# Kernel tuning notes

Measured on AMD Instinct MI355X. Metric: run time of the kernel, lower is better.

## Reference

```python
import jax, jax.numpy as jnp
import numpy as np

N = 8192      # number of tree nodes
IN = 1024     # in_dim
M = 1024      # effective mem_dim = 2 * mem_dim_init
K = 8         # max children (complete 8-ary tree)


def _linear_init(key, out_dim, in_dim):
    k1, k2 = jax.random.split(key)
    s = 1.0 / np.sqrt(in_dim)
    w = jax.random.uniform(k1, (out_dim, in_dim), minval=-s, maxval=s, dtype=jnp.float32)
    b = jax.random.uniform(k2, (out_dim,), minval=-s, maxval=s, dtype=jnp.float32)
    return w, b


def setup_inputs() -> dict:
    key = jax.random.key(0)
    ks = jax.random.split(key, 5)
    w_ioux, b_ioux = _linear_init(ks[0], 3 * M, IN)
    w_iouh, b_iouh = _linear_init(ks[1], 3 * M, M)
    w_fx, b_fx = _linear_init(ks[2], M, IN)
    w_fh, b_fh = _linear_init(ks[3], M, M)
    inputs = jax.random.normal(ks[4], (N, IN), dtype=jnp.float32)
    # Complete K-ary tree: children of node p are p*K+1 .. p*K+K (clipped).
    # Pad with index N, which addresses an always-zero dummy row.
    ch = np.full((N, K), N, dtype=np.int32)
    for j in range(K):
        idx = np.arange(N) * K + 1 + j
        valid = idx < N
        ch[valid, j] = idx[valid]
    return dict(inputs=inputs, children=jnp.asarray(ch),
                w_ioux=w_ioux, b_ioux=b_ioux, w_iouh=w_iouh, b_iouh=b_iouh,
                w_fx=w_fx, b_fx=b_fx, w_fh=w_fh, b_fh=b_fh)


def reference(inputs, children, w_ioux, b_ioux, w_iouh, b_iouh, w_fx, b_fx, w_fh, b_fh):
    # Precompute the input-side projections for all nodes at once.
    iou_x = inputs @ w_ioux.T + b_ioux   # [N, 3M]
    fx_x = inputs @ w_fx.T + b_fx        # [N, M]
    h0 = jnp.zeros((N + 1, M), inputs.dtype)  # row N is the zero pad slot
    c0 = jnp.zeros((N + 1, M), inputs.dtype)

    def step(carry, t):
        h_buf, c_buf = carry
        ch = children[t]           # [K] child indices (pad = N -> zero rows)
        ch_h = h_buf[ch]           # [K, M] real child h's
        ch_c = c_buf[ch]           # [K, M] real child c's
        # Faithful to original: for internal nodes child_c/child_h are SWAPPED,
        # so the 'child_h_sum' and f-gate inputs use the real c's, while the
        # forgotten memory (fc) multiplies the real h's. Leaves: all zeros.
        csum = ch_c.sum(0)                                   # [M]
        iou = iou_x[t] + csum @ w_iouh.T + b_iouh            # [3M]
        i_g, o_g, u_g = jnp.split(iou, 3)
        i_g = jax.nn.sigmoid(i_g)
        o_g = jax.nn.sigmoid(o_g)
        u_g = jnp.tanh(u_g)
        f = jax.nn.sigmoid(ch_c @ w_fh.T + b_fh + fx_x[t])   # [K, M]
        c = i_g * u_g + (f * ch_h).sum(0)                    # [M]
        h = o_g * jnp.tanh(c)
        return (h_buf.at[t].set(h), c_buf.at[t].set(c)), None

    # Children always have larger indices than their parent, so processing
    # t = N-1 .. 0 matches the original reverse-BFS (leaves-first) order.
    order = jnp.arange(N - 1, -1, -1)
    (h_buf, c_buf), _ = jax.lax.scan(step, (h0, c0), order)
    root_h = h_buf[0][None, :]   # [1, M]
    root_c = c_buf[0][None, :]   # [1, M]
    return root_h, root_c
```

## Files before the change

kernel.cpp:

```cpp
#include <hip/hip_runtime.h>

typedef __bf16 bf16x8 __attribute__((ext_vector_type(8)));
typedef __attribute__((ext_vector_type(4))) float f4;

#define AS1 __attribute__((address_space(1)))
#define AS3 __attribute__((address_space(3)))

__device__ __forceinline__ unsigned short f2bf(float f) {
    union { float f; unsigned int u; } x; x.f = f;
    return (unsigned short)((x.u + 0x7fffu + ((x.u >> 16) & 1u)) >> 16);
}
__device__ __forceinline__ float bf2f(unsigned short u) {
    union { unsigned int u; float f; } x; x.u = (unsigned int)u << 16;
    return x.f;
}
__device__ __forceinline__ float fsigm(float x) {
    return __builtin_amdgcn_rcpf(1.f + __expf(-x));
}
__device__ __forceinline__ float ftanh(float x) {
    return 1.f - 2.f * __builtin_amdgcn_rcpf(1.f + __expf(2.f * x));
}
__device__ __forceinline__ void gload_lds16(const unsigned short* g, unsigned short* l) {
    __builtin_amdgcn_global_load_lds((const AS1 unsigned int*)g, (AS3 unsigned int*)l, 16, 0, 0);
}
__device__ __forceinline__ void bar() {
    asm volatile("" ::: "memory");
    __builtin_amdgcn_s_barrier();
    asm volatile("" ::: "memory");
}

__global__ void prep_all_k(const float* __restrict__ inputs, const float* __restrict__ w_ioux,
                           const float* __restrict__ w_fx, const float* __restrict__ w_iouh,
                           const float* __restrict__ w_fh,
                           const float* __restrict__ b_ioux, const float* __restrict__ b_iouh,
                           const float* __restrict__ b_fx, const float* __restrict__ b_fh,
                           unsigned short* __restrict__ Xbf, unsigned short* __restrict__ Wiouxbf,
                           unsigned short* __restrict__ Wfxbf, unsigned short* __restrict__ Whbf,
                           unsigned short* __restrict__ Wfhbf,
                           float* __restrict__ bias_iou, float* __restrict__ bias_f,
                           unsigned short* __restrict__ c_bf, unsigned short* __restrict__ h_bf) {
    int b = blockIdx.x;
    if (b < 16384) {
        int idx = b * 256 + threadIdx.x;
        const float* src; unsigned short* dst; int rel;
        if (idx < 2097152)      { src = inputs; dst = Xbf;     rel = idx; }
        else if (idx < 2883584) { src = w_ioux; dst = Wiouxbf; rel = idx - 2097152; }
        else if (idx < 3145728) { src = w_fx;   dst = Wfxbf;   rel = idx - 2883584; }
        else if (idx < 3932160) { src = w_iouh; dst = Whbf;    rel = idx - 3145728; }
        else                    { src = w_fh;   dst = Wfhbf;   rel = idx - 3932160; }
        float4 v = reinterpret_cast<const float4*>(src)[rel];
        ushort4 o; o.x = f2bf(v.x); o.y = f2bf(v.y); o.z = f2bf(v.z); o.w = f2bf(v.w);
        reinterpret_cast<ushort4*>(dst)[rel] = o;
    } else if (b < 16400) {
        int idx = (b - 16384) * 256 + threadIdx.x;
        if (idx < 3072) bias_iou[idx] = b_ioux[idx] + b_iouh[idx];
        else { int j = idx - 3072; bias_f[j] = b_fx[j] + b_fh[j]; }
    } else {
        int j = (b - 16400) * 256 + threadIdx.x;
        size_t o = (size_t)8192 * 1024 + j;
        c_bf[o] = 0; h_bf[o] = 0;
    }
}

__device__ __forceinline__ void stage_half(const unsigned short* __restrict__ G, int M,
                                           int trow0, int kt, unsigned short* lds_region, int tid) {
#pragma unroll
    for (int ii = 0; ii < 2; ++ii) {
        int c = ii * 512 + tid;
        int r = c >> 3, sl = c & 7;
        int row = min(trow0 + r, M - 1);
        gload_lds16(G + (size_t)row * 1024 + kt * 64 + ((sl ^ (r & 7)) * 8),
                    lds_region + c * 8);
    }
}
__device__ __forceinline__ bf16x8 rdfrag(const unsigned short* region, int rowih, int kslot) {
    return *reinterpret_cast<const bf16x8*>(&region[rowih * 64 + ((kslot ^ (rowih & 7)) * 8)]);
}

#define RD_A(AF, REG, FB)                                                        \
    _Pragma("unroll") for (int f_ = 0; f_ < 4; ++f_)                             \
    _Pragma("unroll") for (int s_ = 0; s_ < 2; ++s_)                             \
        (AF)[f_][s_] = rdfrag((REG), ((FB) + f_) * 16 + fr, s_ * 4 + q);
#define RD_B(BQ, REG, GB)                                                        \
    _Pragma("unroll") for (int g_ = 0; g_ < 2; ++g_)                             \
    _Pragma("unroll") for (int s_ = 0; s_ < 2; ++s_)                             \
        (BQ)[g_][s_] = rdfrag((REG), bcol0 + ((GB) + g_) * 16 + fr, s_ * 4 + q);
#define MF16(FB, GB, AF, BQ)                                                     \
    __builtin_amdgcn_s_setprio(1);                                               \
    _Pragma("unroll") for (int s_ = 0; s_ < 2; ++s_)                             \
    _Pragma("unroll") for (int f_ = 0; f_ < 4; ++f_)                             \
    _Pragma("unroll") for (int g_ = 0; g_ < 2; ++g_)                             \
        acc[(FB) + f_][(GB) + g_] = __builtin_amdgcn_mfma_f32_16x16x32_bf16(     \
            (AF)[f_][s_], (BQ)[g_][s_], acc[(FB) + f_][(GB) + g_], 0, 0, 0);     \
    __builtin_amdgcn_s_setprio(0);

__device__ __forceinline__ void gemm256_core(const unsigned short* __restrict__ Am,
                                             const unsigned short* __restrict__ Bm,
                                             int M, int tm, int tn,
                                             unsigned short* ls, f4 acc[8][4]) {
    const int tid = threadIdx.x;
    const int l = tid & 63, w = tid >> 6;
    const int wm = w >> 2, wn = w & 3;
    const int fr = l & 15, q = l >> 4;
    const int bcol0 = (wn & 1) * 64;
    const int BIGM = 1 << 30;

    unsigned short* S0 = ls;
    unsigned short* S1 = ls + 32768;
    const unsigned short* Ar0 = S0 + wm * 8192;
    const unsigned short* Br0 = S0 + (2 + (wn >> 1)) * 8192;
    const unsigned short* Ar1 = S1 + wm * 8192;
    const unsigned short* Br1 = S1 + (2 + (wn >> 1)) * 8192;

#pragma unroll
    for (int i = 0; i < 8; ++i)
#pragma unroll
        for (int j = 0; j < 4; ++j) acc[i][j] = (f4){0.f, 0.f, 0.f, 0.f};

    stage_half(Am, M, tm,       0, S0 + 0 * 8192, tid);
    stage_half(Am, M, tm + 128, 0, S0 + 1 * 8192, tid);
    stage_half(Bm, BIGM, tn,       0, S0 + 2 * 8192, tid);
    stage_half(Bm, BIGM, tn + 128, 0, S0 + 3 * 8192, tid);
    stage_half(Bm, BIGM, tn,       1, S1 + 2 * 8192, tid);
    stage_half(Bm, BIGM, tn + 128, 1, S1 + 3 * 8192, tid);
    asm volatile("s_waitcnt vmcnt(4)" ::: "memory");
    bar();

    for (int i = 0; i < 8; ++i) {
        bf16x8 afA[4][2], afB[4][2], bq01[2][2], bq23[2][2];
        RD_A(afA, Ar0, 0)
        RD_B(bq01, Br0, 0)
        stage_half(Am, M, tm,       2 * i + 1, S1 + 0 * 8192, tid);
        bar();
        MF16(0, 0, afA, bq01)
        bar();
        RD_B(bq23, Br0, 2)
        stage_half(Am, M, tm + 128, 2 * i + 1, S1 + 1 * 8192, tid);
        bar();
        MF16(0, 2, afA, bq23)
        bar();
        RD_A(afB, Ar0, 4)
        if (i < 7) stage_half(Bm, BIGM, tn,       2 * i + 2, S0 + 2 * 8192, tid);
        bar();
        MF16(4, 2, afB, bq23)
        bar();
        if (i < 7) {
            stage_half(Bm, BIGM, tn + 128, 2 * i + 2, S0 + 3 * 8192, tid);
            asm volatile("s_waitcnt vmcnt(4)" ::: "memory");
        } else {
            asm volatile("s_waitcnt vmcnt(0)" ::: "memory");
        }
        bar();
        MF16(4, 0, afB, bq01)
        bar();
        RD_A(afA, Ar1, 0)
        RD_B(bq01, Br1, 0)
        if (i < 7) stage_half(Am, M, tm,       2 * i + 2, S0 + 0 * 8192, tid);
        bar();
        MF16(0, 0, afA, bq01)
        bar();
        RD_B(bq23, Br1, 2)
        if (i < 7) stage_half(Am, M, tm + 128, 2 * i + 2, S0 + 1 * 8192, tid);
        bar();
        MF16(0, 2, afA, bq23)
        bar();
        RD_A(afB, Ar1, 4)
        if (i < 7) stage_half(Bm, BIGM, tn,       2 * i + 3, S1 + 2 * 8192, tid);
        bar();
        MF16(4, 2, afB, bq23)
        bar();
        if (i < 7) {
            stage_half(Bm, BIGM, tn + 128, 2 * i + 3, S1 + 3 * 8192, tid);
            asm volatile("s_waitcnt vmcnt(4)" ::: "memory");
        } else {
            asm volatile("s_waitcnt vmcnt(0)" ::: "memory");
        }
        bar();
        MF16(4, 0, afB, bq01)
        bar();
    }
}

__global__ __launch_bounds__(512, 2)
void gemm_big_k(const unsigned short* __restrict__ Xbf, const unsigned short* __restrict__ Wioux,
                const unsigned short* __restrict__ Wfx,
                const float* __restrict__ bias_iou, const float* __restrict__ bias_f,
                unsigned short* __restrict__ P_iou, unsigned short* __restrict__ P_f) {
    __shared__ unsigned short ls[65536];
    int b = blockIdx.x;
    b = (b & 7) * 50 + (b >> 3);
    const unsigned short* Bm; unsigned short* Cp; const float* biasp;
    int tm, tn, ldc;
    if (b < 384) {
        int st = b / 24, wt = b % 24;
        tm = ((st >> 2) * 8 + wt / 3) * 256;
        tn = ((st & 3) * 3 + wt % 3) * 256;
        Bm = Wioux; Cp = P_iou; biasp = bias_iou; ldc = 3072;
    } else {
        int bb = b - 384;
        tm = (bb & 3) * 256; tn = (bb >> 2) * 256;
        Bm = Wfx; Cp = P_f; biasp = bias_f; ldc = 1024;
    }
    f4 acc[8][4];
    gemm256_core(Xbf, Bm, 8192, tm, tn, ls, acc);

    const int l = threadIdx.x & 63, w = threadIdx.x >> 6;
    const int wm = w >> 2, wn = w & 3;
    const int fr = l & 15, q = l >> 4;
#pragma unroll
    for (int f = 0; f < 8; ++f)
#pragma unroll
        for (int g = 0; g < 4; ++g) {
            int col = tn + wn * 64 + g * 16 + fr;
            float bv = biasp[col];
#pragma unroll
            for (int r = 0; r < 4; ++r) {
                int row = tm + wm * 128 + f * 16 + q * 4 + r;
                Cp[(size_t)row * ldc + col] = f2bf(acc[f][g][r] + bv);
            }
        }
}

struct LDesc {
    const unsigned short* A;
    const unsigned short* B;
    float* C;
    int M;
    int tiles_n;
    int ldc;
    int tiles_total;
};

__global__ __launch_bounds__(512, 2)
void gemm_lvl_k(LDesc d0, LDesc d1) {
    __shared__ unsigned short ls[65536];
    int b = blockIdx.x;
    LDesc d; int bb;
    if (b < d0.tiles_total) { d = d0; bb = b; }
    else { d = d1; bb = b - d0.tiles_total; }
    const int tm = (bb / d.tiles_n) * 256;
    const int tn = (bb % d.tiles_n) * 256;
    f4 acc[8][4];
    gemm256_core(d.A, d.B, d.M, tm, tn, ls, acc);

    const int l = threadIdx.x & 63, w = threadIdx.x >> 6;
    const int wm = w >> 2, wn = w & 3;
    const int fr = l & 15, q = l >> 4;
#pragma unroll
    for (int f = 0; f < 8; ++f)
#pragma unroll
        for (int g = 0; g < 4; ++g) {
            int col = tn + wn * 64 + g * 16 + fr;
#pragma unroll
            for (int r = 0; r < 4; ++r) {
                int row = tm + wm * 128 + f * 16 + q * 4 + r;
                if (row < d.M) d.C[(size_t)row * d.ldc + col] = acc[f][g][r];
            }
        }
}

__device__ __forceinline__ void gemm_core_db(const unsigned short* __restrict__ A,
                                             const unsigned short* __restrict__ B,
                                             int M, int tile_m, int tile_n, int kb, int nsteps,
                                             unsigned short* lsA, unsigned short* lsB,
                                             f4 acc[4][4]) {
    const int K = 1024;
    const int tid = threadIdx.x;
    const int l = tid & 63, wid = tid >> 6;
    const int wm = wid >> 1, wn = wid & 1;
    const int fr = l & 15, q = l >> 4;

#pragma unroll
    for (int i = 0; i < 4; ++i)
#pragma unroll
        for (int j = 0; j < 4; ++j) acc[i][j] = (f4){0.f, 0.f, 0.f, 0.f};

    const unsigned short* ga[4]; const unsigned short* gb[4];
    unsigned short *la[4], *lb[4];
#pragma unroll
    for (int i = 0; i < 4; ++i) {
        int chunk = i * 256 + tid;
        int row = chunk >> 3, slot = chunk & 7;
        int scol = (slot ^ (row & 7)) * 8;
        ga[i] = A + (size_t)min(tile_m + row, M - 1) * K + kb * 64 + scol;
        gb[i] = B + (size_t)(tile_n + row) * K + kb * 64 + scol;
        la[i] = lsA + chunk * 8;
        lb[i] = lsB + chunk * 8;
    }
#pragma unroll
    for (int i = 0; i < 4; ++i) gload_lds16(ga[i], la[i]);
#pragma unroll
    for (int i = 0; i < 4; ++i) gload_lds16(gb[i], lb[i]);

    int roffA[4], roffB[4];
#pragma unroll
    for (int f = 0; f < 4; ++f) {
        roffA[f] = (wm * 64 + f * 16 + fr) * 64;
        roffB[f] = (wn * 64 + f * 16 + fr) * 64;
    }
    const int sw = fr & 7;
    int cur = 0;
    for (int t = 0; t < nsteps; ++t) {
        if (t < nsteps - 1) {
            int k0 = (t + 1) * 64;
            int nb = (cur ^ 1) * 8192;
#pragma unroll
            for (int i = 0; i < 4; ++i) gload_lds16(ga[i] + k0, la[i] + nb);
#pragma unroll
            for (int i = 0; i < 4; ++i) gload_lds16(gb[i] + k0, lb[i] + nb);
            asm volatile("s_waitcnt vmcnt(8)" ::: "memory");
        } else {
            asm volatile("s_waitcnt vmcnt(0)" ::: "memory");
        }
        __builtin_amdgcn_s_barrier();
        const unsigned short* bA = lsA + cur * 8192;
        const unsigned short* bB = lsB + cur * 8192;
        bf16x8 af[4][2], bq[4][2];
#pragma unroll
        for (int f = 0; f < 4; ++f)
#pragma unroll
            for (int s = 0; s < 2; ++s) {
                int sl = ((s * 4 + q) ^ sw) * 8;
                af[f][s] = *reinterpret_cast<const bf16x8*>(&bA[roffA[f] + sl]);
                bq[f][s] = *reinterpret_cast<const bf16x8*>(&bB[roffB[f] + sl]);
            }
#pragma unroll
        for (int s = 0; s < 2; ++s)
#pragma unroll
            for (int i = 0; i < 4; ++i)
#pragma unroll
                for (int j = 0; j < 4; ++j)
                    acc[i][j] = __builtin_amdgcn_mfma_f32_16x16x32_bf16(af[i][s], bq[j][s], acc[i][j], 0, 0, 0);
        __builtin_amdgcn_s_barrier();
        cur ^= 1;
    }
}

__global__ void leaf_act_k(const unsigned short* __restrict__ P_iou,
                           unsigned short* __restrict__ h_bf, unsigned short* __restrict__ c_bf) {
    int idx = blockIdx.x * blockDim.x + threadIdx.x;
    int t = 1024 + (idx >> 8);
    int j = (idx & 255) * 4;
    const unsigned short* p = P_iou + (size_t)t * 3072 + j;
    ushort4 pi = *reinterpret_cast<const ushort4*>(p);
    ushort4 po = *reinterpret_cast<const ushort4*>(p + 1024);
    ushort4 pu = *reinterpret_cast<const ushort4*>(p + 2048);
    ushort4 cb, hb;
    float c0, c1, c2, c3;
    c0 = fsigm(bf2f(pi.x)) * ftanh(bf2f(pu.x)); hb.x = f2bf(fsigm(bf2f(po.x)) * ftanh(c0)); cb.x = f2bf(c0);
    c1 = fsigm(bf2f(pi.y)) * ftanh(bf2f(pu.y)); hb.y = f2bf(fsigm(bf2f(po.y)) * ftanh(c1)); cb.y = f2bf(c1);
    c2 = fsigm(bf2f(pi.z)) * ftanh(bf2f(pu.z)); hb.z = f2bf(fsigm(bf2f(po.z)) * ftanh(c2)); cb.z = f2bf(c2);
    c3 = fsigm(bf2f(pi.w)) * ftanh(bf2f(pu.w)); hb.w = f2bf(fsigm(bf2f(po.w)) * ftanh(c3)); cb.w = f2bf(c3);
    size_t o = (size_t)t * 1024 + j;
    *reinterpret_cast<ushort4*>(c_bf + o) = cb;
    *reinterpret_cast<ushort4*>(h_bf + o) = hb;
}

__device__ __forceinline__ void csum_dev(const unsigned short* __restrict__ c_bf,
                                         unsigned short* __restrict__ csum_bf, int lo, int w) {
    int tt = w >> 8, j = (w & 255) * 4;
    int t = lo + tt;
    size_t base = (size_t)(t * 8 + 1) * 1024 + j;
    float s0 = 0.f, s1 = 0.f, s2 = 0.f, s3 = 0.f;
#pragma unroll
    for (int k = 0; k < 8; ++k) {
        ushort4 v = *reinterpret_cast<const ushort4*>(c_bf + base + (size_t)k * 1024);
        s0 += bf2f(v.x); s1 += bf2f(v.y); s2 += bf2f(v.z); s3 += bf2f(v.w);
    }
    ushort4 o; o.x = f2bf(s0); o.y = f2bf(s1); o.z = f2bf(s2); o.w = f2bf(s3);
    *reinterpret_cast<ushort4*>(csum_bf + (size_t)t * 1024 + j) = o;
}

__global__ void csum_k(const unsigned short* __restrict__ c_bf, unsigned short* __restrict__ csum_bf,
                       int lo, int n) {
    int w = blockIdx.x * blockDim.x + threadIdx.x;
    if (w < n * 256) csum_dev(c_bf, csum_bf, lo, w);
}

__global__ void node_update_k(const unsigned short* __restrict__ P_iou,
                              const unsigned short* __restrict__ P_f,
                              const float* __restrict__ out_iouh, const float* __restrict__ out_f,
                              unsigned short* __restrict__ h_bf, unsigned short* __restrict__ c_bf,
                              float* __restrict__ out, int lo, int n) {
    int w = blockIdx.x * blockDim.x + threadIdx.x;
    if (w >= n * 256) return;
    int tt = w >> 8, j = (w & 255) * 4;
    int t = lo + tt;
    const unsigned short* p = P_iou + (size_t)t * 3072 + j;
    ushort4 pi4 = *reinterpret_cast<const ushort4*>(p);
    ushort4 po4 = *reinterpret_cast<const ushort4*>(p + 1024);
    ushort4 pu4 = *reinterpret_cast<const ushort4*>(p + 2048);
    const float* oi = out_iouh + (size_t)tt * 3072 + j;
    f4 oii = *reinterpret_cast<const f4*>(oi);
    f4 oio = *reinterpret_cast<const f4*>(oi + 1024);
    f4 oiu = *reinterpret_cast<const f4*>(oi + 2048);
    ushort4 pf4 = *reinterpret_cast<const ushort4*>(P_f + (size_t)t * 1024 + j);
    float pf[4] = {bf2f(pf4.x), bf2f(pf4.y), bf2f(pf4.z), bf2f(pf4.w)};
    float a[4], og[4];
    a[0] = fsigm(bf2f(pi4.x) + oii[0]) * ftanh(bf2f(pu4.x) + oiu[0]);
    a[1] = fsigm(bf2f(pi4.y) + oii[1]) * ftanh(bf2f(pu4.y) + oiu[1]);
    a[2] = fsigm(bf2f(pi4.z) + oii[2]) * ftanh(bf2f(pu4.z) + oiu[2]);
    a[3] = fsigm(bf2f(pi4.w) + oii[3]) * ftanh(bf2f(pu4.w) + oiu[3]);
    og[0] = fsigm(bf2f(po4.x) + oio[0]);
    og[1] = fsigm(bf2f(po4.y) + oio[1]);
    og[2] = fsigm(bf2f(po4.z) + oio[2]);
    og[3] = fsigm(bf2f(po4.w) + oio[3]);
#pragma unroll
    for (int k = 0; k < 8; ++k) {
        f4 fo = *reinterpret_cast<const f4*>(out_f + (size_t)(tt * 8 + k) * 1024 + j);
        ushort4 hc = *reinterpret_cast<const ushort4*>(h_bf + (size_t)(t * 8 + 1 + k) * 1024 + j);
        a[0] += fsigm(pf[0] + fo[0]) * bf2f(hc.x);
        a[1] += fsigm(pf[1] + fo[1]) * bf2f(hc.y);
        a[2] += fsigm(pf[2] + fo[2]) * bf2f(hc.z);
        a[3] += fsigm(pf[3] + fo[3]) * bf2f(hc.w);
    }
    float h0 = og[0] * ftanh(a[0]);
    float h1 = og[1] * ftanh(a[1]);
    float h2 = og[2] * ftanh(a[2]);
    float h3 = og[3] * ftanh(a[3]);
    size_t o = (size_t)t * 1024 + j;
    ushort4 cb; cb.x = f2bf(a[0]); cb.y = f2bf(a[1]); cb.z = f2bf(a[2]); cb.w = f2bf(a[3]);
    ushort4 hb; hb.x = f2bf(h0); hb.y = f2bf(h1); hb.z = f2bf(h2); hb.w = f2bf(h3);
    *reinterpret_cast<ushort4*>(c_bf + o) = cb;
    *reinterpret_cast<ushort4*>(h_bf + o) = hb;
    if (t == 0) {
        f4 hv = {h0, h1, h2, h3};
        f4 cv = {a[0], a[1], a[2], a[3]};
        *reinterpret_cast<f4*>(out + j) = hv;
        *reinterpret_cast<f4*>(out + 1024 + j) = cv;
    }
}

__global__ __launch_bounds__(256)
void gemm_tail_k(const unsigned short* __restrict__ csum_lvl,
                 const unsigned short* __restrict__ cchild,
                 const unsigned short* __restrict__ Whbf, const unsigned short* __restrict__ Wfhbf,
                 float* __restrict__ part_iouh, float* __restrict__ part_f, int n) {
    __shared__ unsigned short lsA[16384];
    __shared__ unsigned short lsB[16384];
    int b = blockIdx.x;
    const unsigned short* A; const unsigned short* Bw; float* C;
    int M, ldc, tm, tn, split;
    if (b < 96) {
        split = b & 3; int tile = b >> 2;
        A = csum_lvl; Bw = Whbf; M = n; ldc = 3072; tm = 0; tn = tile * 128;
        C = part_iouh + (size_t)split * 64 * 3072;
    } else {
        int bb = b - 96;
        split = bb & 3; int tile = bb >> 2;
        A = cchild; Bw = Wfhbf; M = 8 * n; ldc = 1024;
        tm = (tile >> 3) * 128; tn = (tile & 7) * 128;
        C = part_f + (size_t)split * 512 * 1024;
    }
    f4 acc[4][4];
    gemm_core_db(A, Bw, M, tm, tn, split * 4, 4, lsA, lsB, acc);

    const int l = threadIdx.x & 63, wid = threadIdx.x >> 6;
    const int wm = wid >> 1, wn = wid & 1;
    const int fr = l & 15, q = l >> 4;
#pragma unroll
    for (int i = 0; i < 4; ++i)
#pragma unroll
        for (int j = 0; j < 4; ++j) {
            int col = tn + wn * 64 + fr + j * 16;
#pragma unroll
            for (int r = 0; r < 4; ++r) {
                int row = tm + wm * 64 + q * 4 + i * 16 + r;
                if (row < M) C[(size_t)row * ldc + col] = acc[i][j][r];
            }
        }
}

__global__ void node_update_tail_k(const unsigned short* __restrict__ P_iou,
                                   const unsigned short* __restrict__ P_f,
                                   const float* __restrict__ part_iouh,
                                   const float* __restrict__ part_f,
                                   unsigned short* __restrict__ h_bf, unsigned short* __restrict__ c_bf,
                                   float* __restrict__ out, int lo, int n) {
    int w = blockIdx.x * blockDim.x + threadIdx.x;
    if (w >= n * 256) return;
    int tt = w >> 8, j = (w & 255) * 4;
    int t = lo + tt;
    f4 oii = {0.f, 0.f, 0.f, 0.f}, oio = oii, oiu = oii;
#pragma unroll
    for (int s = 0; s < 4; ++s) {
        const float* base = part_iouh + (size_t)s * 64 * 3072 + (size_t)tt * 3072 + j;
        oii += *reinterpret_cast<const f4*>(base);
        oio += *reinterpret_cast<const f4*>(base + 1024);
        oiu += *reinterpret_cast<const f4*>(base + 2048);
    }
    const unsigned short* p = P_iou + (size_t)t * 3072 + j;
    ushort4 pi4 = *reinterpret_cast<const ushort4*>(p);
    ushort4 po4 = *reinterpret_cast<const ushort4*>(p + 1024);
    ushort4 pu4 = *reinterpret_cast<const ushort4*>(p + 2048);
    ushort4 pf4 = *reinterpret_cast<const ushort4*>(P_f + (size_t)t * 1024 + j);
    float pf[4] = {bf2f(pf4.x), bf2f(pf4.y), bf2f(pf4.z), bf2f(pf4.w)};
    float a[4], og[4];
    a[0] = fsigm(bf2f(pi4.x) + oii[0]) * ftanh(bf2f(pu4.x) + oiu[0]);
    a[1] = fsigm(bf2f(pi4.y) + oii[1]) * ftanh(bf2f(pu4.y) + oiu[1]);
    a[2] = fsigm(bf2f(pi4.z) + oii[2]) * ftanh(bf2f(pu4.z) + oiu[2]);
    a[3] = fsigm(bf2f(pi4.w) + oii[3]) * ftanh(bf2f(pu4.w) + oiu[3]);
    og[0] = fsigm(bf2f(po4.x) + oio[0]);
    og[1] = fsigm(bf2f(po4.y) + oio[1]);
    og[2] = fsigm(bf2f(po4.z) + oio[2]);
    og[3] = fsigm(bf2f(po4.w) + oio[3]);
#pragma unroll
    for (int k = 0; k < 8; ++k) {
        f4 fo = {0.f, 0.f, 0.f, 0.f};
#pragma unroll
        for (int s = 0; s < 4; ++s)
            fo += *reinterpret_cast<const f4*>(part_f + (size_t)s * 512 * 1024 +
                                               (size_t)(tt * 8 + k) * 1024 + j);
        ushort4 hc = *reinterpret_cast<const ushort4*>(h_bf + (size_t)(t * 8 + 1 + k) * 1024 + j);
        a[0] += fsigm(pf[0] + fo[0]) * bf2f(hc.x);
        a[1] += fsigm(pf[1] + fo[1]) * bf2f(hc.y);
        a[2] += fsigm(pf[2] + fo[2]) * bf2f(hc.z);
        a[3] += fsigm(pf[3] + fo[3]) * bf2f(hc.w);
    }
    float h0 = og[0] * ftanh(a[0]);
    float h1 = og[1] * ftanh(a[1]);
    float h2 = og[2] * ftanh(a[2]);
    float h3 = og[3] * ftanh(a[3]);
    size_t o = (size_t)t * 1024 + j;
    ushort4 cb; cb.x = f2bf(a[0]); cb.y = f2bf(a[1]); cb.z = f2bf(a[2]); cb.w = f2bf(a[3]);
    ushort4 hb; hb.x = f2bf(h0); hb.y = f2bf(h1); hb.z = f2bf(h2); hb.w = f2bf(h3);
    *reinterpret_cast<ushort4*>(c_bf + o) = cb;
    *reinterpret_cast<ushort4*>(h_bf + o) = hb;
    if (t == 0) {
        f4 hv = {h0, h1, h2, h3};
        f4 cv = {a[0], a[1], a[2], a[3]};
        *reinterpret_cast<f4*>(out + j) = hv;
        *reinterpret_cast<f4*>(out + 1024 + j) = cv;
    }
}

extern "C" void kernel_launch(void* const* d_in, const int* in_sizes, int n_in,
                              void* d_out, int out_size, void* d_ws, size_t ws_size,
                              hipStream_t stream) {
    const float* inputs = (const float*)d_in[0];
    const float* w_ioux = (const float*)d_in[2];
    const float* b_ioux = (const float*)d_in[3];
    const float* w_iouh = (const float*)d_in[4];
    const float* b_iouh = (const float*)d_in[5];
    const float* w_fx   = (const float*)d_in[6];
    const float* b_fx   = (const float*)d_in[7];
    const float* w_fh   = (const float*)d_in[8];
    const float* b_fh   = (const float*)d_in[9];
    float* out = (float*)d_out;

    char* ws = (char*)d_ws;
    size_t off = 0;
    auto alloc = [&](size_t bytes) -> void* {
        void* p = ws + off;
        off += (bytes + 255) & ~(size_t)255;
        return p;
    };
    unsigned short* Xbf     = (unsigned short*)alloc((size_t)8192 * 1024 * 2);
    unsigned short* Wiouxbf = (unsigned short*)alloc((size_t)3072 * 1024 * 2);
    unsigned short* Wfxbf   = (unsigned short*)alloc((size_t)1024 * 1024 * 2);
    unsigned short* Whbf    = (unsigned short*)alloc((size_t)3072 * 1024 * 2);
    unsigned short* Wfhbf   = (unsigned short*)alloc((size_t)1024 * 1024 * 2);
    float* bias_iou         = (float*)alloc((size_t)3072 * 4);
    float* bias_f           = (float*)alloc((size_t)1024 * 4);
    unsigned short* P_iou   = (unsigned short*)alloc((size_t)8192 * 3072 * 2);
    unsigned short* P_f     = (unsigned short*)alloc((size_t)1024 * 1024 * 2);
    unsigned short* c_bf    = (unsigned short*)alloc((size_t)8193 * 1024 * 2);
    unsigned short* h_bf    = (unsigned short*)alloc((size_t)8193 * 1024 * 2);
    unsigned short* csum_bf = (unsigned short*)alloc((size_t)1024 * 1024 * 2);
    float* out_iouh         = (float*)alloc((size_t)512 * 3072 * 4);
    float* out_f            = (float*)alloc((size_t)4096 * 1024 * 4);
    float* part_iouh        = (float*)alloc((size_t)4 * 64 * 3072 * 4);
    float* part_f           = (float*)alloc((size_t)4 * 512 * 1024 * 4);

    prep_all_k<<<dim3(16404), dim3(256), 0, stream>>>(
        inputs, w_ioux, w_fx, w_iouh, w_fh, b_ioux, b_iouh, b_fx, b_fh,
        Xbf, Wiouxbf, Wfxbf, Whbf, Wfhbf, bias_iou, bias_f, c_bf, h_bf);

    gemm_big_k<<<dim3(400), dim3(512), 0, stream>>>(Xbf, Wiouxbf, Wfxbf,
                                                    bias_iou, bias_f, P_iou, P_f);
    leaf_act_k<<<dim3(7168), dim3(256), 0, stream>>>(P_iou, h_bf, c_bf);
    csum_k<<<dim3(896), dim3(256), 0, stream>>>(c_bf, csum_bf, 128, 896);

    {
        const int lo = 585, n = 439;
        LDesc d0, d1;
        d0.A = csum_bf + (size_t)lo * 1024; d0.B = Whbf; d0.C = out_iouh;
        d0.M = n; d0.tiles_n = 12; d0.ldc = 3072; d0.tiles_total = 2 * 12;
        d1.A = c_bf + (size_t)(lo * 8 + 1) * 1024; d1.B = Wfhbf; d1.C = out_f;
        d1.M = 8 * n; d1.tiles_n = 4; d1.ldc = 1024; d1.tiles_total = 14 * 4;
        gemm_lvl_k<<<dim3(d0.tiles_total + d1.tiles_total), dim3(512), 0, stream>>>(d0, d1);
        node_update_k<<<dim3(n), dim3(256), 0, stream>>>(
            P_iou, P_f, out_iouh, out_f, h_bf, c_bf, out, lo, n);
    }
    {
        const int lo = 73, n = 512;
        csum_k<<<dim3(55), dim3(256), 0, stream>>>(c_bf, csum_bf, 73, 55);
        LDesc d0, d1;
        d0.A = csum_bf + (size_t)lo * 1024; d0.B = Whbf; d0.C = out_iouh;
        d0.M = n; d0.tiles_n = 12; d0.ldc = 3072; d0.tiles_total = 2 * 12;
        d1.A = c_bf + (size_t)(lo * 8 + 1) * 1024; d1.B = Wfhbf; d1.C = out_f;
        d1.M = 8 * n; d1.tiles_n = 4; d1.ldc = 1024; d1.tiles_total = 16 * 4;
        gemm_lvl_k<<<dim3(d0.tiles_total + d1.tiles_total), dim3(512), 0, stream>>>(d0, d1);
        node_update_k<<<dim3(n), dim3(256), 0, stream>>>(
            P_iou, P_f, out_iouh, out_f, h_bf, c_bf, out, lo, n);
    }
    const int T_LO[3] = {9, 1, 0};
    const int T_N[3]  = {64, 8, 1};
    for (int lv = 0; lv < 3; ++lv) {
        int lo = T_LO[lv], n = T_N[lv];
        csum_k<<<dim3(n), dim3(256), 0, stream>>>(c_bf, csum_bf, lo, n);
        int fm_tiles = (8 * n + 127) / 128;
        int nblk = 96 + fm_tiles * 8 * 4;
        gemm_tail_k<<<dim3(nblk), dim3(256), 0, stream>>>(
            csum_bf + (size_t)lo * 1024, c_bf + (size_t)(lo * 8 + 1) * 1024,
            Whbf, Wfhbf, part_iouh, part_f, n);
        node_update_tail_k<<<dim3(n), dim3(256), 0, stream>>>(
            P_iou, P_f, part_iouh, part_f, h_bf, c_bf, out, lo, n);
    }
    (void)in_sizes; (void)n_in; (void)out_size; (void)ws_size;
}
```

Before: 214.5 us.

## Fuse leaf activation with child c-sum and retile level GEMMs to 128x128

Merges the leaf activation kernel and the first child-sum kernel into one launch, so each parent block computes its 8 leaf children's c/h and sums c in registers without re-reading c from memory. Only nodes 1024..8192 are actually needed as leaves here, with node 1024 handled by an extra block. The level GEMMs switch from 256x256 tiles with 512 threads to 128x128 double-buffered tiles with 256 threads. This gives many more blocks for the two big tree levels and improves CU fill, in exchange for less operand reuse per tile. Leaf nodes 1025..8191 are now handled only through their parents' blocks.

```diff
diff --git a/kernel.cpp b/kernel.cpp
--- a/kernel.cpp
+++ b/kernel.cpp
@@ -221,44 +221,6 @@
         }
 }
 
-struct LDesc {
-    const unsigned short* A;
-    const unsigned short* B;
-    float* C;
-    int M;
-    int tiles_n;
-    int ldc;
-    int tiles_total;
-};
-
-__global__ __launch_bounds__(512, 2)
-void gemm_lvl_k(LDesc d0, LDesc d1) {
-    __shared__ unsigned short ls[65536];
-    int b = blockIdx.x;
-    LDesc d; int bb;
-    if (b < d0.tiles_total) { d = d0; bb = b; }
-    else { d = d1; bb = b - d0.tiles_total; }
-    const int tm = (bb / d.tiles_n) * 256;
-    const int tn = (bb % d.tiles_n) * 256;
-    f4 acc[8][4];
-    gemm256_core(d.A, d.B, d.M, tm, tn, ls, acc);
-
-    const int l = threadIdx.x & 63, w = threadIdx.x >> 6;
-    const int wm = w >> 2, wn = w & 3;
-    const int fr = l & 15, q = l >> 4;
-#pragma unroll
-    for (int f = 0; f < 8; ++f)
-#pragma unroll
-        for (int g = 0; g < 4; ++g) {
-            int col = tn + wn * 64 + g * 16 + fr;
-#pragma unroll
-            for (int r = 0; r < 4; ++r) {
-                int row = tm + wm * 128 + f * 16 + q * 4 + r;
-                if (row < d.M) d.C[(size_t)row * d.ldc + col] = acc[f][g][r];
-            }
-        }
-}
-
 __device__ __forceinline__ void gemm_core_db(const unsigned short* __restrict__ A,
                                              const unsigned short* __restrict__ B,
                                              int M, int tile_m, int tile_n, int kb, int nsteps,
@@ -336,24 +298,56 @@
     }
 }
 
-__global__ void leaf_act_k(const unsigned short* __restrict__ P_iou,
-                           unsigned short* __restrict__ h_bf, unsigned short* __restrict__ c_bf) {
-    int idx = blockIdx.x * blockDim.x + threadIdx.x;
-    int t = 1024 + (idx >> 8);
-    int j = (idx & 255) * 4;
-    const unsigned short* p = P_iou + (size_t)t * 3072 + j;
-    ushort4 pi = *reinterpret_cast<const ushort4*>(p);
-    ushort4 po = *reinterpret_cast<const ushort4*>(p + 1024);
-    ushort4 pu = *reinterpret_cast<const ushort4*>(p + 2048);
-    ushort4 cb, hb;
-    float c0, c1, c2, c3;
-    c0 = fsigm(bf2f(pi.x)) * ftanh(bf2f(pu.x)); hb.x = f2bf(fsigm(bf2f(po.x)) * ftanh(c0)); cb.x = f2bf(c0);
-    c1 = fsigm(bf2f(pi.y)) * ftanh(bf2f(pu.y)); hb.y = f2bf(fsigm(bf2f(po.y)) * ftanh(c1)); cb.y = f2bf(c1);
-    c2 = fsigm(bf2f(pi.z)) * ftanh(bf2f(pu.z)); hb.z = f2bf(fsigm(bf2f(po.z)) * ftanh(c2)); cb.z = f2bf(c2);
-    c3 = fsigm(bf2f(pi.w)) * ftanh(bf2f(pu.w)); hb.w = f2bf(fsigm(bf2f(po.w)) * ftanh(c3)); cb.w = f2bf(c3);
-    size_t o = (size_t)t * 1024 + j;
-    *reinterpret_cast<ushort4*>(c_bf + o) = cb;
-    *reinterpret_cast<ushort4*>(h_bf + o) = hb;
+__global__ void leafact_csum_k(const unsigned short* __restrict__ P_iou,
+                               unsigned short* __restrict__ h_bf, unsigned short* __restrict__ c_bf,
+                               unsigned short* __restrict__ csum_bf) {
+    int b = blockIdx.x;
+    int j = threadIdx.x * 4;
+    if (b < 896) {
+        int p = 128 + b;
+        float s0 = 0.f, s1 = 0.f, s2 = 0.f, s3 = 0.f;
+#pragma unroll
+        for (int k = 0; k < 8; ++k) {
+            int t = p * 8 + 1 + k;
+            const unsigned short* pp = P_iou + (size_t)t * 3072 + j;
+            ushort4 pi = *reinterpret_cast<const ushort4*>(pp);
+            ushort4 po = *reinterpret_cast<const ushort4*>(pp + 1024);
+            ushort4 pu = *reinterpret_cast<const ushort4*>(pp + 2048);
+            float c0 = fsigm(bf2f(pi.x)) * ftanh(bf2f(pu.x));
+            float c1 = fsigm(bf2f(pi.y)) * ftanh(bf2f(pu.y));
+            float c2 = fsigm(bf2f(pi.z)) * ftanh(bf2f(pu.z));
+            float c3 = fsigm(bf2f(pi.w)) * ftanh(bf2f(pu.w));
+            ushort4 cb, hb;
+            cb.x = f2bf(c0); hb.x = f2bf(fsigm(bf2f(po.x)) * ftanh(c0));
+            cb.y = f2bf(c1); hb.y = f2bf(fsigm(bf2f(po.y)) * ftanh(c1));
+            cb.z = f2bf(c2); hb.z = f2bf(fsigm(bf2f(po.z)) * ftanh(c2));
+            cb.w = f2bf(c3); hb.w = f2bf(fsigm(bf2f(po.w)) * ftanh(c3));
+            size_t o = (size_t)t * 1024 + j;
+            *reinterpret_cast<ushort4*>(c_bf + o) = cb;
+            *reinterpret_cast<ushort4*>(h_bf + o) = hb;
+            s0 += c0; s1 += c1; s2 += c2; s3 += c3;
+        }
+        ushort4 sv; sv.x = f2bf(s0); sv.y = f2bf(s1); sv.z = f2bf(s2); sv.w = f2bf(s3);
+        *reinterpret_cast<ushort4*>(csum_bf + (size_t)p * 1024 + j) = sv;
+    } else {
+        const int t = 1024;
+        const unsigned short* pp = P_iou + (size_t)t * 3072 + j;
+        ushort4 pi = *reinterpret_cast<const ushort4*>(pp);
+        ushort4 po = *reinterpret_cast<const ushort4*>(pp + 1024);
+        ushort4 pu = *reinterpret_cast<const ushort4*>(pp + 2048);
+        float c0 = fsigm(bf2f(pi.x)) * ftanh(bf2f(pu.x));
+        float c1 = fsigm(bf2f(pi.y)) * ftanh(bf2f(pu.y));
+        float c2 = fsigm(bf2f(pi.z)) * ftanh(bf2f(pu.z));
+        float c3 = fsigm(bf2f(pi.w)) * ftanh(bf2f(pu.w));
+        ushort4 cb, hb;
+        cb.x = f2bf(c0); hb.x = f2bf(fsigm(bf2f(po.x)) * ftanh(c0));
+        cb.y = f2bf(c1); hb.y = f2bf(fsigm(bf2f(po.y)) * ftanh(c1));
+        cb.z = f2bf(c2); hb.z = f2bf(fsigm(bf2f(po.z)) * ftanh(c2));
+        cb.w = f2bf(c3); hb.w = f2bf(fsigm(bf2f(po.w)) * ftanh(c3));
+        size_t o = (size_t)t * 1024 + j;
+        *reinterpret_cast<ushort4*>(c_bf + o) = cb;
+        *reinterpret_cast<ushort4*>(h_bf + o) = hb;
+    }
 }
 
 __device__ __forceinline__ void csum_dev(const unsigned short* __restrict__ c_bf,
@@ -431,6 +425,45 @@
     }
 }
 
+struct GDesc {
+    const unsigned short* A;
+    const unsigned short* B;
+    float* C;
+    int M;
+    int ldc;
+    int tiles_n;
+    int tiles_total;
+};
+
+__global__ __launch_bounds__(256)
+void gemm_dual_k(GDesc d0, GDesc d1) {
+    __shared__ unsigned short lsA[16384];
+    __shared__ unsigned short lsB[16384];
+    int b = blockIdx.x;
+    GDesc d; int bb;
+    if (b < d0.tiles_total) { d = d0; bb = b; }
+    else { d = d1; bb = b - d0.tiles_total; }
+    const int tile_m = (bb / d.tiles_n) * 128;
+    const int tile_n = (bb % d.tiles_n) * 128;
+    f4 acc[4][4];
+    gemm_core_db(d.A, d.B, d.M, tile_m, tile_n, 0, 16, lsA, lsB, acc);
+
+    const int l = threadIdx.x & 63, wid = threadIdx.x >> 6;
+    const int wm = wid >> 1, wn = wid & 1;
+    const int fr = l & 15, q = l >> 4;
+#pragma unroll
+    for (int i = 0; i < 4; ++i)
+#pragma unroll
+        for (int j = 0; j < 4; ++j) {
+            int col = tile_n + wn * 64 + fr + j * 16;
+#pragma unroll
+            for (int r = 0; r < 4; ++r) {
+                int row = tile_m + wm * 64 + q * 4 + i * 16 + r;
+                if (row < d.M) d.C[(size_t)row * d.ldc + col] = acc[i][j][r];
+            }
+        }
+}
+
 __global__ __launch_bounds__(256)
 void gemm_tail_k(const unsigned short* __restrict__ csum_lvl,
                  const unsigned short* __restrict__ cchild,
@@ -578,29 +611,32 @@
 
     gemm_big_k<<<dim3(400), dim3(512), 0, stream>>>(Xbf, Wiouxbf, Wfxbf,
                                                     bias_iou, bias_f, P_iou, P_f);
-    leaf_act_k<<<dim3(7168), dim3(256), 0, stream>>>(P_iou, h_bf, c_bf);
-    csum_k<<<dim3(896), dim3(256), 0, stream>>>(c_bf, csum_bf, 128, 896);
+    leafact_csum_k<<<dim3(897), dim3(256), 0, stream>>>(P_iou, h_bf, c_bf, csum_bf);
 
     {
         const int lo = 585, n = 439;
-        LDesc d0, d1;
+        GDesc d0, d1;
         d0.A = csum_bf + (size_t)lo * 1024; d0.B = Whbf; d0.C = out_iouh;
-        d0.M = n; d0.tiles_n = 12; d0.ldc = 3072; d0.tiles_total = 2 * 12;
+        d0.M = n; d0.ldc = 3072; d0.tiles_n = 24;
+        d0.tiles_total = ((n + 127) / 128) * 24;
         d1.A = c_bf + (size_t)(lo * 8 + 1) * 1024; d1.B = Wfhbf; d1.C = out_f;
-        d1.M = 8 * n; d1.tiles_n = 4; d1.ldc = 1024; d1.tiles_total = 14 * 4;
-        gemm_lvl_k<<<dim3(d0.tiles_total + d1.tiles_total), dim3(512), 0, stream>>>(d0, d1);
+        d1.M = 8 * n; d1.ldc = 1024; d1.tiles_n = 8;
+        d1.tiles_total = ((8 * n + 127) / 128) * 8;
+        gemm_dual_k<<<dim3(d0.tiles_total + d1.tiles_total), dim3(256), 0, stream>>>(d0, d1);
         node_update_k<<<dim3(n), dim3(256), 0, stream>>>(
             P_iou, P_f, out_iouh, out_f, h_bf, c_bf, out, lo, n);
     }
     {
         const int lo = 73, n = 512;
         csum_k<<<dim3(55), dim3(256), 0, stream>>>(c_bf, csum_bf, 73, 55);
-        LDesc d0, d1;
+        GDesc d0, d1;
         d0.A = csum_bf + (size_t)lo * 1024; d0.B = Whbf; d0.C = out_iouh;
-        d0.M = n; d0.tiles_n = 12; d0.ldc = 3072; d0.tiles_total = 2 * 12;
+        d0.M = n; d0.ldc = 3072; d0.tiles_n = 24;
+        d0.tiles_total = ((n + 127) / 128) * 24;
         d1.A = c_bf + (size_t)(lo * 8 + 1) * 1024; d1.B = Wfhbf; d1.C = out_f;
-        d1.M = 8 * n; d1.tiles_n = 4; d1.ldc = 1024; d1.tiles_total = 16 * 4;
-        gemm_lvl_k<<<dim3(d0.tiles_total + d1.tiles_total), dim3(512), 0, stream>>>(d0, d1);
+        d1.M = 8 * n; d1.ldc = 1024; d1.tiles_n = 8;
+        d1.tiles_total = ((8 * n + 127) / 128) * 8;
+        gemm_dual_k<<<dim3(d0.tiles_total + d1.tiles_total), dim3(256), 0, stream>>>(d0, d1);
         node_update_k<<<dim3(n), dim3(256), 0, stream>>>(
             P_iou, P_f, out_iouh, out_f, h_bf, c_bf, out, lo, n);
     }
```

Result: faster. 199.7 us (-6.9%).
